# Kernel tuning notes

Measured on AMD Instinct MI355X. Metric: run time of the kernel, lower is better.

The kernel has to match this reference:

```python
import jax, jax.numpy as jnp
import numpy as np

HIDDEN = 2048
N_HEADS = 16
N_KV = 8
HEAD_DIM = 128
EPS = 1e-6
THETA = 1000000.0
T = 2048


def _rmsnorm(x, w):
    # x: [T, h, D]; normalize over last dim
    var = jnp.mean(x * x, axis=-1, keepdims=True)
    return x * jax.lax.rsqrt(var + EPS) * w


def _rope(x, positions):
    # neox-style rotate-half, rotary_dim == head_dim
    D = x.shape[-1]
    inv_freq = 1.0 / (THETA ** (jnp.arange(0, D, 2, dtype=jnp.float32) / D))  # [D/2]
    freqs = positions.astype(jnp.float32)[:, None] * inv_freq  # [T, D/2]
    cos = jnp.cos(freqs)[:, None, :]  # [T, 1, D/2]
    sin = jnp.sin(freqs)[:, None, :]
    x1, x2 = jnp.split(x, 2, axis=-1)
    return jnp.concatenate([x1 * cos - x2 * sin, x2 * cos + x1 * sin], axis=-1)


def setup_inputs() -> dict:
    key = jax.random.key(0)
    ks = jax.random.split(key, 7)
    s = 0.02
    return {
        "positions": jnp.arange(T, dtype=jnp.int32),
        "hidden_states": jax.random.normal(ks[0], (T, HIDDEN), dtype=jnp.float32),
        "wq": jax.random.normal(ks[1], (HIDDEN, N_HEADS * HEAD_DIM), dtype=jnp.float32) * s,
        "wk": jax.random.normal(ks[2], (HIDDEN, N_KV * HEAD_DIM), dtype=jnp.float32) * s,
        "wv": jax.random.normal(ks[3], (HIDDEN, N_KV * HEAD_DIM), dtype=jnp.float32) * s,
        "wo": jax.random.normal(ks[4], (N_HEADS * HEAD_DIM, HIDDEN), dtype=jnp.float32) * s,
        "q_norm_w": jnp.ones((HEAD_DIM,), dtype=jnp.float32),
        "k_norm_w": jnp.ones((HEAD_DIM,), dtype=jnp.float32),
    }


def reference(positions, hidden_states, wq, wk, wv, wo, q_norm_w, k_norm_w):
    q = (hidden_states @ wq).reshape(-1, N_HEADS, HEAD_DIM)
    k = (hidden_states @ wk).reshape(-1, N_KV, HEAD_DIM)
    v = (hidden_states @ wv).reshape(-1, N_KV, HEAD_DIM)
    q = _rmsnorm(q, q_norm_w)
    k = _rmsnorm(k, k_norm_w)
    q = _rope(q, positions)
    k = _rope(k, positions)
    # GQA: expand kv heads
    rep = N_HEADS // N_KV
    k = jnp.repeat(k, rep, axis=1)  # [T, H, D]
    v = jnp.repeat(v, rep, axis=1)
    scale = HEAD_DIM ** -0.5
    scores = jnp.einsum('qhd,khd->hqk', q, k) * scale  # [H, T, T]
    tq = q.shape[0]
    causal = jnp.tril(jnp.ones((tq, tq), dtype=bool))
    scores = jnp.where(causal[None], scores, jnp.finfo(scores.dtype).min)
    probs = jax.nn.softmax(scores, axis=-1)
    o = jnp.einsum('hqk,khd->qhd', probs, v).reshape(tq, N_HEADS * HEAD_DIM)
    return o @ wo
```

## Files before the change

kernel.cpp:

```cpp
#include <hip/hip_runtime.h>
#include <cstdint>

#define TT 2048
#define NH 16
#define NKV 8
#define HD 128
#define SCALE_L2E 0.12751743f
#define SM_M2 16.5f

typedef unsigned short u16;
typedef unsigned int u32;
typedef u16 u16x8 __attribute__((ext_vector_type(8)));
typedef u32 u32x2 __attribute__((ext_vector_type(2)));
typedef __bf16 bf16x8 __attribute__((ext_vector_type(8)));
typedef float f32x4 __attribute__((ext_vector_type(4)));
typedef float f32x16 __attribute__((ext_vector_type(16)));

__device__ inline u16 f2bf(float x){
  u32 u = __builtin_bit_cast(u32, x);
  u = (u + 0x7fffu + ((u >> 16) & 1u)) >> 16;
  return (u16)u;
}
__device__ inline float bf2f(u16 h){
  return __builtin_bit_cast(float, (u32)h << 16);
}
__device__ inline bf16x8 as_bf(u16x8 v){ return __builtin_bit_cast(bf16x8, v); }

__device__ inline void gl_lds16(const void* g, void* l){
  typedef __attribute__((address_space(1))) const void gv_t;
  typedef __attribute__((address_space(3))) void lv_t;
  __builtin_amdgcn_global_load_lds((gv_t*)g, (lv_t*)l, 16, 0, 0);
}

__device__ inline void tc_body(const float* __restrict__ in, u16* __restrict__ out,
                               int R, int C, int bx, int by, int tid, float (*tile)[65]){
  #pragma unroll
  for (int i = 0; i < 4; ++i){
    int idx = i * 256 + tid;
    int r = idx >> 4, c4 = (idx & 15) * 4;
    float4 v = *(const float4*)&in[(size_t)(by + r) * C + bx + c4];
    tile[r][c4] = v.x; tile[r][c4 + 1] = v.y; tile[r][c4 + 2] = v.z; tile[r][c4 + 3] = v.w;
  }
  __syncthreads();
  #pragma unroll
  for (int i = 0; i < 2; ++i){
    int idx = i * 256 + tid;
    int cc = idx >> 3, s8 = (idx & 7) * 8;
    u16x8 o;
    #pragma unroll
    for (int j = 0; j < 8; ++j) o[j] = f2bf(tile[s8 + j][cc]);
    *(u16x8*)&out[(size_t)(bx + cc) * R + by + s8] = o;
  }
}

__global__ void prep_weights(const float* __restrict__ hidden, const float* __restrict__ wq,
                             const float* __restrict__ wk, const float* __restrict__ wv,
                             const float* __restrict__ wo, u16* __restrict__ hs,
                             u16* __restrict__ Wqkv, u16* __restrict__ Wo){
  __shared__ float tile[64][65];
  int b = blockIdx.x, tid = threadIdx.x;
  if (b < 2048){
    int i = b * 256 + tid;
    const float4* p = (const float4*)(hidden + (size_t)i * 8);
    float4 a = p[0], bb = p[1];
    u16x8 o = { f2bf(a.x), f2bf(a.y), f2bf(a.z), f2bf(a.w),
                f2bf(bb.x), f2bf(bb.y), f2bf(bb.z), f2bf(bb.w) };
    *(u16x8*)(hs + (size_t)i * 8) = o;
  } else if (b < 3072){
    int bb = b - 2048;
    tc_body(wq, Wqkv, 2048, 2048, (bb & 31) * 64, (bb >> 5) * 64, tid, tile);
  } else if (b < 3584){
    int bb = b - 3072;
    tc_body(wk, Wqkv + (size_t)2048 * 2048, 2048, 1024, (bb & 15) * 64, (bb >> 4) * 64, tid, tile);
  } else if (b < 4096){
    int bb = b - 3584;
    tc_body(wv, Wqkv + (size_t)3072 * 2048, 2048, 1024, (bb & 15) * 64, (bb >> 4) * 64, tid, tile);
  } else {
    int bb = b - 4096;
    tc_body(wo, Wo, 2048, 2048, (bb & 31) * 64, (bb >> 5) * 64, tid, tile);
  }
}

__global__ void prep_qkv(const u16* __restrict__ QKV, const int* __restrict__ pos,
                         const float* __restrict__ qw, const float* __restrict__ kw,
                         u16* __restrict__ Qr, u16* __restrict__ Kr, u16* __restrict__ Vt){
  __shared__ u16 tile[64][72];
  int b = blockIdx.x, tid = threadIdx.x;
  if (b < 12288){
    int gw = (b * 256 + tid) >> 6;
    int ln = tid & 63;
    int t = gw / 24, idx = gw % 24;
    if (t >= TT) return;
    bool isq = idx < NH;
    int head = isq ? idx : idx - NH;
    const u16* src = QKV + (size_t)t * 4096 + (isq ? head * HD : 2048 + head * HD);
    const float* wgt = isq ? qw : kw;
    float x0 = bf2f(src[ln]), x1 = bf2f(src[ln + 64]);
    float ss = x0 * x0 + x1 * x1;
    #pragma unroll
    for (int off = 32; off; off >>= 1) ss += __shfl_xor(ss, off);
    float r = rsqrtf(ss * (1.0f / 128.0f) + 1e-6f);
    float xn0 = x0 * r * wgt[ln], xn1 = x1 * r * wgt[ln + 64];
    float inv = exp2f(-(float)ln * 0.311430758895690f);
    float ang = (float)pos[t] * inv;
    float c = cosf(ang), s = sinf(ang);
    float o0 = xn0 * c - xn1 * s;
    float o1 = xn1 * c + xn0 * s;
    u16* dst = isq ? (Qr + (size_t)t * 2048 + head * HD) : (Kr + (size_t)t * 1024 + head * HD);
    dst[ln]      = f2bf(o0);
    dst[ln + 64] = f2bf(o1);
  } else {
    int bb = b - 12288;
    int t0 = (bb & 31) * 64;
    int d0 = ((bb >> 5) & 1) * 64;
    int kh = bb >> 6;
    #pragma unroll
    for (int it = 0; it < 2; ++it){
      int idx = it * 256 + tid;
      int tr = idx >> 3, seg = idx & 7;
      *(u16x8*)&tile[tr][seg * 8] =
        *(const u16x8*)(QKV + (size_t)(t0 + tr) * 4096 + 3072 + kh * HD + d0 + seg * 8);
    }
    __syncthreads();
    #pragma unroll
    for (int it = 0; it < 2; ++it){
      int idx = it * 256 + tid;
      int dr = idx >> 3, seg = idx & 7;
      u16x8 v;
      #pragma unroll
      for (int j = 0; j < 8; j++) v[j] = tile[seg * 8 + j][dr];
      *(u16x8*)(Vt + ((size_t)kh * HD + d0 + dr) * 2048 + t0 + seg * 8) = v;
    }
  }
}

#define MF16(mmp, af, bf)                                                            \
  do {                                                                               \
    __builtin_amdgcn_s_setprio(1);                                                   \
    _Pragma("unroll") for (int m2 = 0; m2 < 2; m2++)                                 \
    _Pragma("unroll") for (int nn = 0; nn < 4; nn++)                                 \
    _Pragma("unroll") for (int kk = 0; kk < 2; kk++)                                 \
      acc[(mmp)*2 + m2][nn] = __builtin_amdgcn_mfma_f32_16x16x32_bf16(               \
        (af)[m2*2 + kk], (bf)[nn*2 + kk], acc[(mmp)*2 + m2][nn], 0, 0, 0);           \
    __builtin_amdgcn_s_setprio(0);                                                   \
  } while (0)

template<bool F32OUT>
__global__ __launch_bounds__(512, 2) void gemm8ph(const u16* __restrict__ A, const u16* __restrict__ B,
                                                  void* __restrict__ Cv, int Klen,
                                                  int lda, int ldb, int ldc, size_t zstride){
  extern __shared__ u16 smem[];
  const int tid = threadIdx.x;
  const int wv = tid >> 6, ln = tid & 63;
  const int lg = ln >> 4, l15 = ln & 15;
  const int wr = wv >> 2, wc = wv & 3;
  const int nbx = gridDim.x;
  const int orig = blockIdx.x + nbx * blockIdx.y;
  const int cpx = (nbx * gridDim.y) >> 3;
  const int swz = (orig & 7) * cpx + (orig >> 3);
  const int m0 = (swz / nbx) * 128, n0 = (swz % nbx) * 256;
  const int Kofs = blockIdx.z * Klen;
  const u16* Ab0 = A + (size_t)m0 * lda + Kofs;
  const u16* Bb0 = B + (size_t)n0 * ldb + Kofs;
  f32x4 acc[4][4] = {};

  auto stageA = [&](int buf, int kt, int c){
    int idx = c * 512 + tid;
    int r = idx >> 3, sl = idx & 7, g = sl ^ (r & 7);
    gl_lds16(Ab0 + (size_t)kt * 64 + (size_t)r * lda + g * 8,
             smem + buf * 24576 + (c * 512 + wv * 64) * 8);
  };
  auto stageB = [&](int buf, int kt, int q){
    int idx = q * 512 + tid;
    int r = idx >> 3, sl = idx & 7, g = sl ^ (r & 7);
    gl_lds16(Bb0 + (size_t)kt * 64 + (size_t)r * ldb + g * 8,
             smem + buf * 24576 + 8192 + (q * 512 + wv * 64) * 8);
  };
  auto ldA = [&](const u16* bufA, int mmp, bf16x8* af){
    #pragma unroll
    for (int m2 = 0; m2 < 2; m2++)
      #pragma unroll
      for (int kk = 0; kk < 2; kk++){
        int ra = wr * 64 + (mmp * 2 + m2) * 16 + l15;
        int sl = (kk * 4 + lg) ^ (ra & 7);
        af[m2 * 2 + kk] = as_bf(*(const u16x8*)&bufA[(ra * 8 + sl) * 8]);
      }
  };
  auto ldB = [&](const u16* bufB, bf16x8* bf){
    #pragma unroll
    for (int nn = 0; nn < 4; nn++)
      #pragma unroll
      for (int kk = 0; kk < 2; kk++){
        int cb = wc * 64 + nn * 16 + l15;
        int sl = (kk * 4 + lg) ^ (cb & 7);
        bf[nn * 2 + kk] = as_bf(*(const u16x8*)&bufB[(cb * 8 + sl) * 8]);
      }
  };

  const int nk = Klen / 64;
  #pragma unroll
  for (int c = 0; c < 2; ++c) stageA(0, 0, c);
  #pragma unroll
  for (int q = 0; q < 4; ++q) stageB(0, 0, q);
  #pragma unroll
  for (int c = 0; c < 2; ++c) stageA(1, 1, c);
  #pragma unroll
  for (int q = 0; q < 4; ++q) stageB(1, 1, q);
  asm volatile("s_waitcnt vmcnt(6)" ::: "memory");
  asm volatile("s_barrier" ::: "memory");

  bf16x8 af[4], bf[8];
  for (int u = 0; u < nk; u += 2){
    const int b0 = u % 3, b1 = (u + 1) % 3, b2 = (u + 2) % 3;
    const u16* A0 = smem + b0 * 24576;  const u16* B0 = A0 + 8192;
    const u16* A1 = smem + b1 * 24576;  const u16* B1 = A1 + 8192;
    const bool st = (u + 2 < nk);
    ldA(A0, 0, af); ldB(B0, bf);
    if (st){ stageA(b2, u + 2, 0); stageA(b2, u + 2, 1); stageB(b2, u + 2, 0); }
    asm volatile("s_barrier" ::: "memory");
    asm volatile("s_waitcnt lgkmcnt(0)" ::: "memory");
    __builtin_amdgcn_sched_barrier(0);
    MF16(0, af, bf);
    asm volatile("s_barrier" ::: "memory");
    ldA(A0, 1, af);
    if (st){ stageB(b2, u + 2, 1); stageB(b2, u + 2, 2); stageB(b2, u + 2, 3); }
    if (st) asm volatile("s_waitcnt vmcnt(6)" ::: "memory");
    else    asm volatile("s_waitcnt vmcnt(0)" ::: "memory");
    asm volatile("s_barrier" ::: "memory");
    asm volatile("s_waitcnt lgkmcnt(0)" ::: "memory");
    __builtin_amdgcn_sched_barrier(0);
    MF16(1, af, bf);
    asm volatile("s_barrier" ::: "memory");
    ldA(A1, 0, af); ldB(B1, bf);
    if (st){ stageA(b0, u + 3, 0); stageA(b0, u + 3, 1); stageB(b0, u + 3, 0); }
    asm volatile("s_barrier" ::: "memory");
    asm volatile("s_waitcnt lgkmcnt(0)" ::: "memory");
    __builtin_amdgcn_sched_barrier(0);
    MF16(0, af, bf);
    asm volatile("s_barrier" ::: "memory");
    ldA(A1, 1, af);
    if (st){ stageB(b0, u + 3, 1); stageB(b0, u + 3, 2); stageB(b0, u + 3, 3); }
    if (st) asm volatile("s_waitcnt vmcnt(6)" ::: "memory");
    asm volatile("s_barrier" ::: "memory");
    asm volatile("s_waitcnt lgkmcnt(0)" ::: "memory");
    __builtin_amdgcn_sched_barrier(0);
    MF16(1, af, bf);
    asm volatile("s_barrier" ::: "memory");
  }
  #pragma unroll
  for (int mm = 0; mm < 4; mm++)
    #pragma unroll
    for (int nn = 0; nn < 4; nn++){
      int grow0 = m0 + wr * 64 + mm * 16 + lg * 4;
      int gcol  = n0 + wc * 64 + nn * 16 + l15;
      #pragma unroll
      for (int r = 0; r < 4; r++){
        float v = acc[mm][nn][r];
        if (F32OUT) ((float*)Cv + blockIdx.z * zstride)[(size_t)(grow0 + r) * ldc + gcol] = v;
        else        ((u16*)Cv)[(size_t)(grow0 + r) * ldc + gcol] = f2bf(v);
      }
    }
}

__global__ __launch_bounds__(512, 2) void gemm_n128(const u16* __restrict__ A, const u16* __restrict__ B,
                                                    float* __restrict__ C, int Klen,
                                                    int lda, int ldb, int ldc){
  extern __shared__ u16 smem[];
  const int tid = threadIdx.x;
  const int wv = tid >> 6, ln = tid & 63;
  const int lg = ln >> 4, l15 = ln & 15;
  const int wr = wv >> 2, wc = wv & 3;
  const int nbx = gridDim.x;
  const int orig = blockIdx.x + nbx * blockIdx.y;
  const int cpx = (nbx * gridDim.y) >> 3;
  const int swz = (orig & 7) * cpx + (orig >> 3);
  const int m0 = (swz / nbx) * 128, n0 = (swz % nbx) * 128;
  const u16* Ab0 = A + (size_t)m0 * lda;
  const u16* Bb0 = B + (size_t)n0 * ldb;
  f32x4 acc[4][2] = {};

  auto stage4 = [&](int buf, int kt){
    #pragma unroll
    for (int c = 0; c < 2; ++c){
      int idx = c * 512 + tid;
      int r = idx >> 3, sl = idx & 7, g = sl ^ (r & 7);
      gl_lds16(Ab0 + (size_t)kt * 64 + (size_t)r * lda + g * 8,
               smem + buf * 16384 + (c * 512 + wv * 64) * 8);
    }
    #pragma unroll
    for (int q = 0; q < 2; ++q){
      int idx = q * 512 + tid;
      int r = idx >> 3, sl = idx & 7, g = sl ^ (r & 7);
      gl_lds16(Bb0 + (size_t)kt * 64 + (size_t)r * ldb + g * 8,
               smem + buf * 16384 + 8192 + (q * 512 + wv * 64) * 8);
    }
  };

  const int nk = Klen / 64;
  stage4(0, 0);
  stage4(1, 1);
  asm volatile("s_waitcnt vmcnt(4)" ::: "memory");
  asm volatile("s_barrier" ::: "memory");

  for (int u = 0; u < nk; ++u){
    const u16* A0 = smem + (u % 3) * 16384;
    const u16* B0 = A0 + 8192;
    const bool st = (u + 2 < nk);
    bf16x8 af[8], bf[4];
    #pragma unroll
    for (int mm = 0; mm < 4; mm++)
      #pragma unroll
      for (int kk = 0; kk < 2; kk++){
        int ra = wr * 64 + mm * 16 + l15;
        int sl = (kk * 4 + lg) ^ (ra & 7);
        af[mm * 2 + kk] = as_bf(*(const u16x8*)&A0[(ra * 8 + sl) * 8]);
      }
    #pragma unroll
    for (int nn = 0; nn < 2; nn++)
      #pragma unroll
      for (int kk = 0; kk < 2; kk++){
        int cb = wc * 32 + nn * 16 + l15;
        int sl = (kk * 4 + lg) ^ (cb & 7);
        bf[nn * 2 + kk] = as_bf(*(const u16x8*)&B0[(cb * 8 + sl) * 8]);
      }
    if (st) stage4((u + 2) % 3, u + 2);
    if (st) asm volatile("s_waitcnt vmcnt(4)" ::: "memory");
    else    asm volatile("s_waitcnt vmcnt(0)" ::: "memory");
    asm volatile("s_barrier" ::: "memory");
    asm volatile("s_waitcnt lgkmcnt(0)" ::: "memory");
    __builtin_amdgcn_sched_barrier(0);
    __builtin_amdgcn_s_setprio(1);
    #pragma unroll
    for (int mm = 0; mm < 4; mm++)
      #pragma unroll
      for (int nn = 0; nn < 2; nn++)
        #pragma unroll
        for (int kk = 0; kk < 2; kk++)
          acc[mm][nn] = __builtin_amdgcn_mfma_f32_16x16x32_bf16(
            af[mm * 2 + kk], bf[nn * 2 + kk], acc[mm][nn], 0, 0, 0);
    __builtin_amdgcn_s_setprio(0);
    asm volatile("s_barrier" ::: "memory");
  }
  #pragma unroll
  for (int mm = 0; mm < 4; mm++)
    #pragma unroll
    for (int nn = 0; nn < 2; nn++){
      int grow0 = m0 + wr * 64 + mm * 16 + lg * 4;
      int gcol  = n0 + wc * 32 + nn * 16 + l15;
      #pragma unroll
      for (int r = 0; r < 4; r++)
        C[(size_t)(grow0 + r) * ldc + gcol] = acc[mm][nn][r];
    }
}

__global__ __launch_bounds__(512, 4) void attn(const u16* __restrict__ Qr, const u16* __restrict__ Kr,
                                               const u16* __restrict__ Vt, u16* __restrict__ O){
  extern __shared__ u16 smem[];
  u16* Karea = smem;
  u16* Varea = smem + 16384;
  u16* Parea = smem + 32768;
  const int h = blockIdx.y, kh = h >> 1;
  const int qc = (h < 8) ? blockIdx.x : 31 - blockIdx.x;
  const int tid = threadIdx.x, wv = tid >> 6, ln = tid & 63;
  const bool isS = wv < 4;
  const int role = wv & 3;
  const int qw = role & 1, jp = role >> 1;
  const int q5 = ln & 31, hb = ln >> 5;
  const int nit = qc + 1;
  const int xr = (q5 & 3) << 1;

  auto stage = [&](int i){
    if (i + 1 < nit){
      u16* Kd = Karea + ((i + 1) & 1) * 8192;
      #pragma unroll
      for (int j = 0; j < 2; ++j){
        int lin = j * 512 + tid;
        int tok = lin >> 4, seg = lin & 15;
        gl_lds16(Kr + (size_t)((i + 1) * 64 + tok) * 1024 + kh * HD + (seg ^ (tok & 7)) * 8,
                 Kd + (j * 512 + wv * 64) * 8);
      }
    }
    if (i < nit){
      u16* Vd = Varea + (i & 1) * 8192;
      #pragma unroll
      for (int j = 0; j < 2; ++j){
        int lin = j * 512 + tid;
        int d = lin >> 3, sl = lin & 7;
        gl_lds16(Vt + (size_t)kh * HD * 2048 + (size_t)d * 2048 + i * 64 + (sl ^ (d & 7)) * 8,
                 Vd + (j * 512 + wv * 64) * 8);
      }
    }
  };

  #pragma unroll
  for (int j = 0; j < 2; ++j){
    int lin = j * 512 + tid;
    int tok = lin >> 4, seg = lin & 15;
    gl_lds16(Kr + (size_t)tok * 1024 + kh * HD + (seg ^ (tok & 7)) * 8,
             Karea + (j * 512 + wv * 64) * 8);
  }

  const u16x8 ones_u = {0x3f80, 0x3f80, 0x3f80, 0x3f80, 0x3f80, 0x3f80, 0x3f80, 0x3f80};
  const bf16x8 onesf = as_bf(ones_u);

  if (isS){
    bf16x8 qf[8];
    {
      const u16* qp = Qr + (size_t)(qc * 64 + qw * 32 + q5) * 2048 + h * HD + hb * 8;
      #pragma unroll
      for (int s = 0; s < 8; ++s) qf[s] = as_bf(*(const u16x8*)(qp + s * 16));
    }
    for (int i = 0; i <= nit; ++i){
      __syncthreads();
      stage(i);
      const int t = 2 * i + jp;
      const int D0 = 32 * t - 64 * qc - 32 * qw;
      const bool act = (i < nit) && (D0 <= 0);
      if (act){
        const u16* Kb = Karea + (i & 1) * 8192;
        const int tokIdx = 32 * jp + q5;
        f32x16 ca = {}, cb = {};
        __builtin_amdgcn_s_setprio(1);
        #pragma unroll
        for (int s = 0; s < 4; ++s){
          int seg = (2 * s + hb) ^ (q5 & 7);
          bf16x8 kf = as_bf(*(const u16x8*)&Kb[tokIdx * 128 + seg * 8]);
          ca = __builtin_amdgcn_mfma_f32_32x32x16_bf16(kf, qf[s], ca, 0, 0, 0);
        }
        #pragma unroll
        for (int s = 4; s < 8; ++s){
          int seg = (2 * s + hb) ^ (q5 & 7);
          bf16x8 kf = as_bf(*(const u16x8*)&Kb[tokIdx * 128 + seg * 8]);
          cb = __builtin_amdgcn_mfma_f32_32x32x16_bf16(kf, qf[s], cb, 0, 0, 0);
        }
        __builtin_amdgcn_s_setprio(0);
        f32x16 c = ca + cb;
        const bool diag = (D0 == 0);
        u32 pk[8];
        #pragma unroll
        for (int j = 0; j < 8; ++j){
          float pv[2];
          #pragma unroll
          for (int e = 0; e < 2; ++e){
            int r = 2 * j + e;
            int tok = (r & 3) + 8 * (r >> 2) + 4 * hb;
            float x = c[r] * SCALE_L2E - SM_M2;
            if (diag && tok > q5) x = -1e30f;
            pv[e] = exp2f(x);
          }
          pk[j] = (__builtin_bit_cast(u32, pv[0]) >> 16) |
                  (__builtin_bit_cast(u32, pv[1]) & 0xffff0000u);
        }
        u16* Pq = Parea + (i & 1) * 4096 + role * 1024 + q5 * 32;
        *(u32x2*)&Pq[((hb + 0) ^ xr) * 4] = u32x2{pk[0], pk[1]};
        *(u32x2*)&Pq[((hb + 2) ^ xr) * 4] = u32x2{pk[2], pk[3]};
        *(u32x2*)&Pq[((hb + 4) ^ xr) * 4] = u32x2{pk[4], pk[5]};
        *(u32x2*)&Pq[((hb + 6) ^ xr) * 4] = u32x2{pk[6], pk[7]};
      }
    }
    __syncthreads();
    __syncthreads();
  } else {
    f32x16 acc[4] = {};
    f32x16 asum = {};
    for (int i = 0; i <= nit; ++i){
      __syncthreads();
      stage(i);
      const int t = 2 * (i - 1) + jp;
      const int D0 = 32 * t - 64 * qc - 32 * qw;
      const bool act = (i >= 1) && (D0 <= 0);
      if (act){
        const u16* Pq = Parea + ((i - 1) & 1) * 4096 + role * 1024 + q5 * 32;
        bf16x8 pf0 = as_bf(*(const u16x8*)&Pq[((2 * hb + 0) ^ xr) * 4]);
        bf16x8 pf1 = as_bf(*(const u16x8*)&Pq[((2 * hb + 4) ^ xr) * 4]);
        const u16* Vb = Varea + ((i - 1) & 1) * 8192;
        __builtin_amdgcn_s_setprio(1);
        asum = __builtin_amdgcn_mfma_f32_32x32x16_bf16(pf0, onesf, asum, 0, 0, 0);
        asum = __builtin_amdgcn_mfma_f32_32x32x16_bf16(pf1, onesf, asum, 0, 0, 0);
        #pragma unroll
        for (int dblk = 0; dblk < 4; ++dblk){
          int d = dblk * 32 + q5;
          bf16x8 v0 = as_bf(*(const u16x8*)&Vb[d * 64 + ((4 * jp + 0 + hb) ^ (d & 7)) * 8]);
          bf16x8 v1 = as_bf(*(const u16x8*)&Vb[d * 64 + ((4 * jp + 2 + hb) ^ (d & 7)) * 8]);
          acc[dblk] = __builtin_amdgcn_mfma_f32_32x32x16_bf16(pf0, v0, acc[dblk], 0, 0, 0);
          acc[dblk] = __builtin_amdgcn_mfma_f32_32x32x16_bf16(pf1, v1, acc[dblk], 0, 0, 0);
        }
        __builtin_amdgcn_s_setprio(0);
      }
    }
    __syncthreads();
    float* Ls  = (float*)smem;
    float* LsS = (float*)smem + 8192;
    if (jp == 1){
      #pragma unroll
      for (int dblk = 0; dblk < 4; ++dblk)
        #pragma unroll
        for (int r = 0; r < 16; ++r){
          int qrow = (r & 3) + 8 * (r >> 2) + 4 * hb;
          Ls[qw * 4096 + qrow * 128 + dblk * 32 + q5] = acc[dblk][r];
        }
      if (q5 == 0){
        #pragma unroll
        for (int r = 0; r < 16; ++r){
          int qrow = (r & 3) + 8 * (r >> 2) + 4 * hb;
          LsS[qw * 32 + qrow] = asum[r];
        }
      }
    }
    __syncthreads();
    if (jp == 0){
      #pragma unroll
      for (int r = 0; r < 16; ++r){
        int qrow = (r & 3) + 8 * (r >> 2) + 4 * hb;
        float rs = 1.0f / (asum[r] + LsS[qw * 32 + qrow]);
        int qg = qc * 64 + qw * 32 + qrow;
        #pragma unroll
        for (int dblk = 0; dblk < 4; ++dblk){
          float o = (acc[dblk][r] + Ls[qw * 4096 + qrow * 128 + dblk * 32 + q5]) * rs;
          O[(size_t)qg * 2048 + h * HD + dblk * 32 + q5] = f2bf(o);
        }
      }
    }
  }
}

extern "C" void kernel_launch(void* const* d_in, const int* in_sizes, int n_in,
                              void* d_out, int out_size, void* d_ws, size_t ws_size,
                              hipStream_t stream){
  const int*   positions = (const int*)d_in[0];
  const float* hidden    = (const float*)d_in[1];
  const float* wq        = (const float*)d_in[2];
  const float* wk        = (const float*)d_in[3];
  const float* wv        = (const float*)d_in[4];
  const float* wo        = (const float*)d_in[5];
  const float* qw        = (const float*)d_in[6];
  const float* kw        = (const float*)d_in[7];
  float* out = (float*)d_out;

  char* ws = (char*)d_ws;
  u16* hs   = (u16*)ws; ws += (size_t)2048 * 2048 * 2;
  u16* Wqkv = (u16*)ws; ws += (size_t)4096 * 2048 * 2;
  u16* Wo   = (u16*)ws; ws += (size_t)2048 * 2048 * 2;
  u16* QKV  = (u16*)ws; ws += (size_t)2048 * 4096 * 2;
  u16* Qr   = (u16*)ws; ws += (size_t)2048 * 2048 * 2;
  u16* Kr   = (u16*)ws; ws += (size_t)2048 * 1024 * 2;
  u16* Vt   = (u16*)ws; ws += (size_t)8 * 128 * 2048 * 2;
  u16* O    = (u16*)ws;

  prep_weights<<<5120, 256, 0, stream>>>(hidden, wq, wk, wv, wo, hs, Wqkv, Wo);

  gemm8ph<false><<<dim3(16, 16, 1), 512, 147456, stream>>>(hs, Wqkv, QKV, 2048, 2048, 2048, 4096, 0);

  prep_qkv<<<12800, 256, 0, stream>>>(QKV, positions, qw, kw, Qr, Kr, Vt);

  attn<<<dim3(32, 16), 512, 81920, stream>>>(Qr, Kr, Vt, O);

  gemm_n128<<<dim3(16, 16), 512, 98304, stream>>>(O, Wo, out, 2048, 2048, 2048, 2048);
}
```

Baseline: 137.2 us.

## Load K and V fragments directly from global memory in attention

The attention kernel no longer stages K and V tiles into double-buffered LDS with asynchronous global-to-LDS copies. Each wave now reads its K and V fragments straight from global memory inside the MFMA loop. Only the P buffer and the epilogue scratch stay in LDS, so the shared memory request drops to about 33 KB. That frees LDS and may allow more resident blocks. In exchange, the MFMAs now wait on global-load latency with no prefetch, and waves that share a K/V tile each fetch it again through the caches.

```diff
diff --git a/kernel.cpp b/kernel.cpp
--- a/kernel.cpp
+++ b/kernel.cpp
@@ -356,9 +356,7 @@
 __global__ __launch_bounds__(512, 4) void attn(const u16* __restrict__ Qr, const u16* __restrict__ Kr,
                                                const u16* __restrict__ Vt, u16* __restrict__ O){
   extern __shared__ u16 smem[];
-  u16* Karea = smem;
-  u16* Varea = smem + 16384;
-  u16* Parea = smem + 32768;
+  u16* Parea = smem;
   const int h = blockIdx.y, kh = h >> 1;
   const int qc = (h < 8) ? blockIdx.x : 31 - blockIdx.x;
   const int tid = threadIdx.x, wv = tid >> 6, ln = tid & 63;
@@ -369,37 +367,6 @@
   const int nit = qc + 1;
   const int xr = (q5 & 3) << 1;
 
-  auto stage = [&](int i){
-    if (i + 1 < nit){
-      u16* Kd = Karea + ((i + 1) & 1) * 8192;
-      #pragma unroll
-      for (int j = 0; j < 2; ++j){
-        int lin = j * 512 + tid;
-        int tok = lin >> 4, seg = lin & 15;
-        gl_lds16(Kr + (size_t)((i + 1) * 64 + tok) * 1024 + kh * HD + (seg ^ (tok & 7)) * 8,
-                 Kd + (j * 512 + wv * 64) * 8);
-      }
-    }
-    if (i < nit){
-      u16* Vd = Varea + (i & 1) * 8192;
-      #pragma unroll
-      for (int j = 0; j < 2; ++j){
-        int lin = j * 512 + tid;
-        int d = lin >> 3, sl = lin & 7;
-        gl_lds16(Vt + (size_t)kh * HD * 2048 + (size_t)d * 2048 + i * 64 + (sl ^ (d & 7)) * 8,
-                 Vd + (j * 512 + wv * 64) * 8);
-      }
-    }
-  };
-
-  #pragma unroll
-  for (int j = 0; j < 2; ++j){
-    int lin = j * 512 + tid;
-    int tok = lin >> 4, seg = lin & 15;
-    gl_lds16(Kr + (size_t)tok * 1024 + kh * HD + (seg ^ (tok & 7)) * 8,
-             Karea + (j * 512 + wv * 64) * 8);
-  }
-
   const u16x8 ones_u = {0x3f80, 0x3f80, 0x3f80, 0x3f80, 0x3f80, 0x3f80, 0x3f80, 0x3f80};
   const bf16x8 onesf = as_bf(ones_u);
 
@@ -412,25 +379,21 @@
     }
     for (int i = 0; i <= nit; ++i){
       __syncthreads();
-      stage(i);
       const int t = 2 * i + jp;
       const int D0 = 32 * t - 64 * qc - 32 * qw;
       const bool act = (i < nit) && (D0 <= 0);
       if (act){
-        const u16* Kb = Karea + (i & 1) * 8192;
-        const int tokIdx = 32 * jp + q5;
+        const u16* Kg = Kr + (size_t)(i * 64 + 32 * jp + q5) * 1024 + kh * HD + hb * 8;
         f32x16 ca = {}, cb = {};
         __builtin_amdgcn_s_setprio(1);
         #pragma unroll
         for (int s = 0; s < 4; ++s){
-          int seg = (2 * s + hb) ^ (q5 & 7);
-          bf16x8 kf = as_bf(*(const u16x8*)&Kb[tokIdx * 128 + seg * 8]);
+          bf16x8 kf = as_bf(*(const u16x8*)(Kg + s * 16));
           ca = __builtin_amdgcn_mfma_f32_32x32x16_bf16(kf, qf[s], ca, 0, 0, 0);
         }
         #pragma unroll
         for (int s = 4; s < 8; ++s){
-          int seg = (2 * s + hb) ^ (q5 & 7);
-          bf16x8 kf = as_bf(*(const u16x8*)&Kb[tokIdx * 128 + seg * 8]);
+          bf16x8 kf = as_bf(*(const u16x8*)(Kg + s * 16));
           cb = __builtin_amdgcn_mfma_f32_32x32x16_bf16(kf, qf[s], cb, 0, 0, 0);
         }
         __builtin_amdgcn_s_setprio(0);
@@ -465,7 +428,6 @@
     f32x16 asum = {};
     for (int i = 0; i <= nit; ++i){
       __syncthreads();
-      stage(i);
       const int t = 2 * (i - 1) + jp;
       const int D0 = 32 * t - 64 * qc - 32 * qw;
       const bool act = (i >= 1) && (D0 <= 0);
@@ -473,15 +435,15 @@
         const u16* Pq = Parea + ((i - 1) & 1) * 4096 + role * 1024 + q5 * 32;
         bf16x8 pf0 = as_bf(*(const u16x8*)&Pq[((2 * hb + 0) ^ xr) * 4]);
         bf16x8 pf1 = as_bf(*(const u16x8*)&Pq[((2 * hb + 4) ^ xr) * 4]);
-        const u16* Vb = Varea + ((i - 1) & 1) * 8192;
+        const u16* Vg = Vt + (size_t)kh * HD * 2048 + (i - 1) * 64 + (4 * jp + hb) * 8;
         __builtin_amdgcn_s_setprio(1);
         asum = __builtin_amdgcn_mfma_f32_32x32x16_bf16(pf0, onesf, asum, 0, 0, 0);
         asum = __builtin_amdgcn_mfma_f32_32x32x16_bf16(pf1, onesf, asum, 0, 0, 0);
         #pragma unroll
         for (int dblk = 0; dblk < 4; ++dblk){
           int d = dblk * 32 + q5;
-          bf16x8 v0 = as_bf(*(const u16x8*)&Vb[d * 64 + ((4 * jp + 0 + hb) ^ (d & 7)) * 8]);
-          bf16x8 v1 = as_bf(*(const u16x8*)&Vb[d * 64 + ((4 * jp + 2 + hb) ^ (d & 7)) * 8]);
+          bf16x8 v0 = as_bf(*(const u16x8*)(Vg + (size_t)d * 2048));
+          bf16x8 v1 = as_bf(*(const u16x8*)(Vg + (size_t)d * 2048 + 16));
           acc[dblk] = __builtin_amdgcn_mfma_f32_32x32x16_bf16(pf0, v0, acc[dblk], 0, 0, 0);
           acc[dblk] = __builtin_amdgcn_mfma_f32_32x32x16_bf16(pf1, v1, acc[dblk], 0, 0, 0);
         }
@@ -553,7 +515,7 @@
 
   prep_qkv<<<12800, 256, 0, stream>>>(QKV, positions, qw, kw, Qr, Kr, Vt);
 
-  attn<<<dim3(32, 16), 512, 81920, stream>>>(Qr, Kr, Vt, O);
+  attn<<<dim3(32, 16), 512, 33024, stream>>>(Qr, Kr, Vt, O);
 
   gemm_n128<<<dim3(16, 16), 512, 98304, stream>>>(O, Wo, out, 2048, 2048, 2048, 2048);
 }
```

After: 183.6 us. +33.9%, slower.
